# Kernel optimization log

Hardware: AMD Instinct MI355X
Metric: run time of the kernel (lower is better)

The kernel has to match this reference:

```python
import jax, jax.numpy as jnp
import numpy as np

B, L, D = 8, 1024, 1024
H = 16
HD = D // H  # 64
R = 8


def setup_inputs() -> dict:
    key = jax.random.key(0)
    ks = jax.random.split(key, 12)
    s = 1.0 / np.sqrt(D)
    return {
        "x": jax.random.normal(ks[0], (B, L, D), dtype=jnp.float32),
        "Wq": jax.random.normal(ks[1], (D, D), dtype=jnp.float32) * s,
        "bq": jnp.zeros((D,), dtype=jnp.float32),
        "Wk": jax.random.normal(ks[2], (D, D), dtype=jnp.float32) * s,
        "bk": jnp.zeros((D,), dtype=jnp.float32),
        "Wv": jax.random.normal(ks[3], (D, D), dtype=jnp.float32) * s,
        "bv": jnp.zeros((D,), dtype=jnp.float32),
        "Wo": jax.random.normal(ks[4], (D, D), dtype=jnp.float32) * s,
        "bo": jnp.zeros((D,), dtype=jnp.float32),
        "Wrel": jax.random.normal(ks[5], (H, R), dtype=jnp.float32) * (1.0 / np.sqrt(H)),
        "brel": jnp.zeros((R,), dtype=jnp.float32),
    }


def reference(x, Wq, bq, Wk, bk, Wv, bv, Wo, bo, Wrel, brel):
    # Standard MHA with need_weights=True: full [B,H,L,L] attention matrix.
    def heads(t):  # [B,L,D] -> [B,H,L,HD]
        return t.reshape(B, L, H, HD).transpose(0, 2, 1, 3)

    q = heads(x @ Wq + bq)
    k = heads(x @ Wk + bk)
    v = heads(x @ Wv + bv)

    scores = jnp.einsum('bhld,bhmd->bhlm', q, k) / jnp.sqrt(jnp.float32(HD))
    attn = jax.nn.softmax(scores, axis=-1)  # [B,H,L,L]

    ctx = jnp.einsum('bhlm,bhmd->bhld', attn, v)
    ctx = ctx.transpose(0, 2, 1, 3).reshape(B, L, D)
    output = ctx @ Wo + bo  # [B,L,D]

    # head_patterns: mean of attention weights over (L, L) -> [B, H]
    head_patterns = attn.mean(axis=(2, 3))
    relation_scores = head_patterns @ Wrel + brel  # [B,R]
    return output, relation_scores
```

## Files before the change

kernel.cpp:

```cpp
#include <hip/hip_runtime.h>
#include <math.h>

using f32x4  = __attribute__((ext_vector_type(4))) float;
using bf16x8 = __attribute__((ext_vector_type(8))) short;
using us8    = __attribute__((ext_vector_type(8))) unsigned short;
using us4    = __attribute__((ext_vector_type(4))) unsigned short;

static __device__ __forceinline__ unsigned short f32_bf16(float f) {
    unsigned int u = __float_as_uint(f);
    u += 0x7fffu + ((u >> 16) & 1u);
    return (unsigned short)(u >> 16);
}

static __device__ __forceinline__ float fast_exp2(float x) {
    return __builtin_amdgcn_exp2f(x);
}

static __device__ __forceinline__ unsigned int bf16pk(float lo, float hi) {
    unsigned int r;
    asm("v_cvt_pk_bf16_f32 %0, %1, %2" : "=v"(r) : "v"(lo), "v"(hi));
    return r;
}

#define GLOADLDS16(src, dst)                                                          \
    __builtin_amdgcn_global_load_lds(                                                 \
        (const __attribute__((address_space(1))) void*)(src),                         \
        (__attribute__((address_space(3))) void*)(dst), 16, 0, 0)

__global__ __launch_bounds__(256) void conv_x_kernel(const float* __restrict__ x,
                                                     unsigned short* __restrict__ xb) {
    const int i = blockIdx.x * 256 + threadIdx.x;
    const float4 v = ((const float4*)x)[i];
    us4 o;
    o.x = f32_bf16(v.x); o.y = f32_bf16(v.y); o.z = f32_bf16(v.z); o.w = f32_bf16(v.w);
    ((us4*)xb)[i] = o;
}

__global__ __launch_bounds__(256) void conv_wT_kernel(
    const float* __restrict__ Wq, const float* __restrict__ Wk,
    const float* __restrict__ Wv, const float* __restrict__ Wo,
    unsigned short* __restrict__ wqkvT, unsigned short* __restrict__ woT) {
    __shared__ float t[32][33];
    const int z = blockIdx.z;
    const float* W = (z == 0) ? Wq : (z == 1) ? Wk : (z == 2) ? Wv : Wo;
    unsigned short* dst = (z < 3) ? (wqkvT + (size_t)z * 1024 * 1024) : woT;
    const int bx = blockIdx.x * 32, by = blockIdx.y * 32;
    const int tx = threadIdx.x & 31, ty = threadIdx.x >> 5;
#pragma unroll
    for (int i = ty; i < 32; i += 8)
        t[i][tx] = W[(size_t)(by + i) * 1024 + bx + tx];
    __syncthreads();
#pragma unroll
    for (int i = ty; i < 32; i += 8)
        dst[(size_t)(bx + i) * 1024 + by + tx] = f32_bf16(t[tx][i]);
}

template<int MODE>
__global__ __launch_bounds__(256, 2) void gemm_bt_kernel(
    const unsigned short* __restrict__ A, const unsigned short* __restrict__ Bt,
    const float* __restrict__ bias_q, const float* __restrict__ bias_k,
    const float* __restrict__ bias_v,
    unsigned short* __restrict__ qkv, float* __restrict__ cout) {
    constexpr int K = 1024;
    __shared__ unsigned short As[256 * 64];
    __shared__ unsigned short Bs[128 * 64];
    const int tid = threadIdx.x;
    const int wid = tid >> 6, lane = tid & 63;
    const int bm = blockIdx.x * 256, bn = blockIdx.y * 128;
    const int wr = wid >> 1, wc = wid & 1;
    const int l15 = lane & 15, lg = lane >> 4;
    const int srow = lane >> 3;
    const int schunk = (lane & 7) ^ srow;

    f32x4 acc[8][4] = {};

    for (int kt = 0; kt < K / 64; ++kt) {
#pragma unroll
        for (int i = 0; i < 8; ++i) {
            const int li = wid * 8 + i;
            GLOADLDS16(A + (size_t)(bm + li * 8 + srow) * K + kt * 64 + schunk * 8,
                       &As[li * 512]);
        }
#pragma unroll
        for (int i = 0; i < 4; ++i) {
            const int li = wid * 4 + i;
            GLOADLDS16(Bt + (size_t)(bn + li * 8 + srow) * K + kt * 64 + schunk * 8,
                       &Bs[li * 512]);
        }
        __syncthreads();
#pragma unroll
        for (int ks = 0; ks < 2; ++ks) {
            bf16x8 bfr[4];
#pragma unroll
            for (int n = 0; n < 4; ++n) {
                const int row = wc * 64 + n * 16 + l15;
                const int c = (ks * 4 + lg) ^ (row & 7);
                bfr[n] = *(const bf16x8*)&Bs[row * 64 + c * 8];
            }
#pragma unroll
            for (int m = 0; m < 8; ++m) {
                const int row = wr * 128 + m * 16 + l15;
                const int c = (ks * 4 + lg) ^ (row & 7);
                const bf16x8 af = *(const bf16x8*)&As[row * 64 + c * 8];
#pragma unroll
                for (int n = 0; n < 4; ++n)
                    acc[m][n] = __builtin_amdgcn_mfma_f32_16x16x32_bf16(
                        bfr[n], af, acc[m][n], 0, 0, 0);
            }
        }
        __syncthreads();
    }
    if constexpr (MODE == 0) {
        const int which = bn >> 10;
        const int hnb = (bn & 1023) + wc * 64;
        const float* bias = (which == 0) ? bias_q : (which == 1) ? bias_k : bias_v;
        if (which == 2) {
#pragma unroll
            for (int m = 0; m < 8; ++m) {
                const int gm = bm + wr * 128 + m * 16 + l15;
                const int b_ = gm >> 10, li2 = gm & 1023;
#pragma unroll
                for (int n = 0; n < 4; ++n) {
                    const int hn0 = hnb + n * 16 + lg * 4;
                    const float4 bb = *(const float4*)&bias[hn0];
                    const float vv[4] = {acc[m][n][0] + bb.x, acc[m][n][1] + bb.y,
                                         acc[m][n][2] + bb.z, acc[m][n][3] + bb.w};
#pragma unroll
                    for (int r = 0; r < 4; ++r) {
                        const int hn = hn0 + r;
                        qkv[16777216 +
                            ((size_t)(b_ * 16 + (hn >> 6)) * 64 + (hn & 63)) * 1024 +
                            li2] = f32_bf16(vv[r]);
                    }
                }
            }
        } else {
            const float qs = (which == 0) ? 0.125f * 1.44269504088896f : 1.0f;
#pragma unroll
            for (int m = 0; m < 8; ++m) {
                const int gm = bm + wr * 128 + m * 16 + l15;
                const size_t rowbase =
                    (((size_t)which * 128 + (gm >> 10) * 16) * 1024 + (gm & 1023)) * 64;
#pragma unroll
                for (int n = 0; n < 4; ++n) {
                    const int hn0 = hnb + n * 16 + lg * 4;
                    const float4 bb = *(const float4*)&bias[hn0];
                    const unsigned int w01 = bf16pk((acc[m][n][0] + bb.x) * qs,
                                                    (acc[m][n][1] + bb.y) * qs);
                    const unsigned int w23 = bf16pk((acc[m][n][2] + bb.z) * qs,
                                                    (acc[m][n][3] + bb.w) * qs);
                    uint2 t2; t2.x = w01; t2.y = w23;
                    *(uint2*)&qkv[rowbase + (size_t)(hn0 >> 6) * 65536 + (hn0 & 63)] = t2;
                }
            }
        }
    } else {
#pragma unroll
        for (int m = 0; m < 8; ++m) {
            const int gm = bm + wr * 128 + m * 16 + l15;
#pragma unroll
            for (int n = 0; n < 4; ++n) {
                const int gn0 = bn + wc * 64 + n * 16 + lg * 4;
                const float4 bb = *(const float4*)&bias_q[gn0];
                float4 o;
                o.x = acc[m][n][0] + bb.x; o.y = acc[m][n][1] + bb.y;
                o.z = acc[m][n][2] + bb.z; o.w = acc[m][n][3] + bb.w;
                *(float4*)&cout[(size_t)gm * 1024 + gn0] = o;
            }
        }
    }
}

__global__ __launch_bounds__(512) void attn_kernel(
    const unsigned short* __restrict__ qkv, unsigned short* __restrict__ ctx) {
    __shared__ unsigned short Ks[2][4096];
    __shared__ unsigned short VTs[2][4096];
    __shared__ unsigned short Ps[8][1024];
    const int bh = blockIdx.x, qt = blockIdx.y;
    const int b = bh >> 4, h = bh & 15;
    const unsigned short* Qp  = qkv + (size_t)bh * 65536;
    const unsigned short* Kp  = qkv + 8388608  + (size_t)bh * 65536;
    const unsigned short* VTp = qkv + 16777216 + (size_t)bh * 65536;
    const int tid = threadIdx.x, wid = tid >> 6, lane = tid & 63;
    const int l15 = lane & 15, lg = lane >> 4;
    const int q0 = qt * 128 + wid * 16;
    const int srow = lane >> 3;
    const int schunk = (lane & 7) ^ srow;

    bf16x8 qf[2];
#pragma unroll
    for (int ks = 0; ks < 2; ++ks)
        qf[ks] = *(const bf16x8*)(Qp + (size_t)(q0 + l15) * 64 + ks * 32 + lg * 8);

    f32x4 oacc[4] = {};
    float lrow = 0.f;

    int koff[4][2], poff_r[2], poff_w[4];
#pragma unroll
    for (int nf = 0; nf < 4; ++nf)
#pragma unroll
        for (int ks = 0; ks < 2; ++ks) {
            const int row = nf * 16 + l15;
            koff[nf][ks] = row * 64 + (((ks * 4 + lg) ^ (row & 7)) * 8);
        }
#pragma unroll
    for (int ks = 0; ks < 2; ++ks)
        poff_r[ks] = l15 * 64 + (((ks * 4 + lg) ^ (l15 & 7)) * 8);
#pragma unroll
    for (int nf = 0; nf < 4; ++nf) {
        const int cchunk = nf * 2 + (lg >> 1);
        poff_w[nf] = l15 * 64 + ((cchunk ^ (l15 & 7)) * 8) + (lg & 1) * 4;
    }
    unsigned short* Pw = &Ps[wid][0];

#define ATTN_STAGE(KT, BB)                                                            \
    do {                                                                              \
        GLOADLDS16(Kp + (size_t)((KT) * 64 + wid * 8 + srow) * 64 + schunk * 8,       \
                   &Ks[BB][wid * 512]);                                               \
        GLOADLDS16(VTp + (size_t)(wid * 8 + srow) * 1024 + (KT) * 64 + schunk * 8,    \
                   &VTs[BB][wid * 512]);                                              \
    } while (0)

    ATTN_STAGE(0, 0);
    for (int kt = 0; kt < 16; ++kt) {
        const int cur = kt & 1;
        if (kt < 15) {
            ATTN_STAGE(kt + 1, cur ^ 1);
            asm volatile("s_waitcnt vmcnt(2)" ::: "memory");
        } else {
            asm volatile("s_waitcnt vmcnt(0)" ::: "memory");
        }
        __builtin_amdgcn_s_barrier();

        const unsigned short* Kb = &Ks[cur][0];
        const unsigned short* Vb = &VTs[cur][0];

        f32x4 sacc[4] = {};
        __builtin_amdgcn_s_setprio(1);
#pragma unroll
        for (int ks = 0; ks < 2; ++ks)
#pragma unroll
            for (int nf = 0; nf < 4; ++nf) {
                const bf16x8 kf = *(const bf16x8*)&Kb[koff[nf][ks]];
                sacc[nf] = __builtin_amdgcn_mfma_f32_16x16x32_bf16(
                    kf, qf[ks], sacc[nf], 0, 0, 0);
            }
        __builtin_amdgcn_s_setprio(0);

        float rsa = 0.f, rsb = 0.f;
#pragma unroll
        for (int nf = 0; nf < 4; ++nf) {
            const float p0 = fast_exp2(sacc[nf][0]);
            const float p1 = fast_exp2(sacc[nf][1]);
            const float p2 = fast_exp2(sacc[nf][2]);
            const float p3 = fast_exp2(sacc[nf][3]);
            rsa += p0 + p1; rsb += p2 + p3;
            uint2 t; t.x = bf16pk(p0, p1); t.y = bf16pk(p2, p3);
            *(uint2*)&Pw[poff_w[nf]] = t;
        }
        lrow += rsa + rsb;

        __builtin_amdgcn_s_setprio(1);
#pragma unroll
        for (int ks = 0; ks < 2; ++ks) {
            const bf16x8 pf = *(const bf16x8*)&Pw[poff_r[ks]];
#pragma unroll
            for (int nf = 0; nf < 4; ++nf) {
                const bf16x8 vf = *(const bf16x8*)&Vb[koff[nf][ks]];
                oacc[nf] = __builtin_amdgcn_mfma_f32_16x16x32_bf16(
                    vf, pf, oacc[nf], 0, 0, 0);
            }
        }
        __builtin_amdgcn_s_setprio(0);

        __builtin_amdgcn_s_barrier();
    }
#undef ATTN_STAGE

    lrow += __shfl_xor(lrow, 16);
    lrow += __shfl_xor(lrow, 32);
    const float rl = 1.0f / lrow;

#pragma unroll
    for (int nf = 0; nf < 4; ++nf) {
        uint2 t;
        t.x = bf16pk(oacc[nf][0] * rl, oacc[nf][1] * rl);
        t.y = bf16pk(oacc[nf][2] * rl, oacc[nf][3] * rl);
        *(uint2*)&ctx[((size_t)(b * 1024 + q0 + l15)) * 1024 + h * 64 + nf * 16 +
                      lg * 4] = t;
    }
}

__global__ __launch_bounds__(64) void relation_kernel(
    const float* __restrict__ Wrel, const float* __restrict__ brel,
    float* __restrict__ out) {
    const int t = threadIdx.x;
    const int r = t & 7;
    float s = 0.f;
#pragma unroll
    for (int hh = 0; hh < 16; ++hh) s += Wrel[hh * 8 + r];
    out[8 * 1024 * 1024 + t] = s * (1.0f / 1024.0f) + brel[r];
}

extern "C" void kernel_launch(void* const* d_in, const int* in_sizes, int n_in,
                              void* d_out, int out_size, void* d_ws, size_t ws_size,
                              hipStream_t stream) {
    (void)in_sizes; (void)n_in; (void)out_size; (void)ws_size;
    const float* x    = (const float*)d_in[0];
    const float* Wq   = (const float*)d_in[1];
    const float* bq   = (const float*)d_in[2];
    const float* Wk   = (const float*)d_in[3];
    const float* bk   = (const float*)d_in[4];
    const float* Wv   = (const float*)d_in[5];
    const float* bv   = (const float*)d_in[6];
    const float* Wo   = (const float*)d_in[7];
    const float* bo   = (const float*)d_in[8];
    const float* Wrel = (const float*)d_in[9];
    const float* brel = (const float*)d_in[10];
    float* out = (float*)d_out;

    char* ws = (char*)d_ws;
    unsigned short* xb    = (unsigned short*)ws;
    unsigned short* wqkvT = (unsigned short*)(ws + 16777216);
    unsigned short* woT   = (unsigned short*)(ws + 16777216 + 6291456);
    unsigned short* qkv   = (unsigned short*)(ws + 16777216 + 6291456 + 2097152);
    unsigned short* ctx   = xb;

    conv_x_kernel<<<8192, 256, 0, stream>>>(x, xb);
    conv_wT_kernel<<<dim3(32, 32, 4), 256, 0, stream>>>(Wq, Wk, Wv, Wo, wqkvT, woT);
    gemm_bt_kernel<0><<<dim3(32, 24), 256, 0, stream>>>(
        xb, wqkvT, bq, bk, bv, qkv, nullptr);
    attn_kernel<<<dim3(128, 8), 512, 0, stream>>>(qkv, ctx);
    gemm_bt_kernel<1><<<dim3(32, 8), 256, 0, stream>>>(
        ctx, woT, bo, nullptr, nullptr, nullptr, out);
    relation_kernel<<<1, 64, 0, stream>>>(Wrel, brel, out);
}
```

Measured before the change: 162.8 us.

## Process two query sub-tiles per wave in attention to reuse K/V fragments

The attention kernel now runs 4 waves per block instead of 8, and each wave handles 32 query rows as two 16-row sub-tiles. Each K and V^T fragment read from LDS feeds two MFMAs, which halves LDS fragment traffic per unit of compute. Each wave now issues two global-to-LDS loads per stage, so the wait count is raised to match. The cost is more accumulator registers per wave and fewer waves per block, which launch_bounds(256,2) tries to offset by allowing two blocks per CU.

```diff
diff --git a/kernel.cpp b/kernel.cpp
--- a/kernel.cpp
+++ b/kernel.cpp
@@ -171,11 +171,11 @@
     }
 }
 
-__global__ __launch_bounds__(512) void attn_kernel(
+__global__ __launch_bounds__(256, 2) void attn_kernel(
     const unsigned short* __restrict__ qkv, unsigned short* __restrict__ ctx) {
     __shared__ unsigned short Ks[2][4096];
     __shared__ unsigned short VTs[2][4096];
-    __shared__ unsigned short Ps[8][1024];
+    __shared__ unsigned short Ps[4][2][1024];
     const int bh = blockIdx.x, qt = blockIdx.y;
     const int b = bh >> 4, h = bh & 15;
     const unsigned short* Qp  = qkv + (size_t)bh * 65536;
@@ -183,17 +183,20 @@
     const unsigned short* VTp = qkv + 16777216 + (size_t)bh * 65536;
     const int tid = threadIdx.x, wid = tid >> 6, lane = tid & 63;
     const int l15 = lane & 15, lg = lane >> 4;
-    const int q0 = qt * 128 + wid * 16;
+    const int q0 = qt * 128 + wid * 32;
     const int srow = lane >> 3;
     const int schunk = (lane & 7) ^ srow;
 
-    bf16x8 qf[2];
-#pragma unroll
-    for (int ks = 0; ks < 2; ++ks)
-        qf[ks] = *(const bf16x8*)(Qp + (size_t)(q0 + l15) * 64 + ks * 32 + lg * 8);
-
-    f32x4 oacc[4] = {};
-    float lrow = 0.f;
+    bf16x8 qf[2][2];
+#pragma unroll
+    for (int s = 0; s < 2; ++s)
+#pragma unroll
+        for (int ks = 0; ks < 2; ++ks)
+            qf[s][ks] = *(const bf16x8*)(Qp + (size_t)(q0 + s * 16 + l15) * 64 +
+                                         ks * 32 + lg * 8);
+
+    f32x4 oacc[2][4] = {};
+    float lrow[2] = {0.f, 0.f};
 
     int koff[4][2], poff_r[2], poff_w[4];
 #pragma unroll
@@ -211,14 +214,17 @@
         const int cchunk = nf * 2 + (lg >> 1);
         poff_w[nf] = l15 * 64 + ((cchunk ^ (l15 & 7)) * 8) + (lg & 1) * 4;
     }
-    unsigned short* Pw = &Ps[wid][0];
 
 #define ATTN_STAGE(KT, BB)                                                            \
     do {                                                                              \
-        GLOADLDS16(Kp + (size_t)((KT) * 64 + wid * 8 + srow) * 64 + schunk * 8,       \
-                   &Ks[BB][wid * 512]);                                               \
-        GLOADLDS16(VTp + (size_t)(wid * 8 + srow) * 1024 + (KT) * 64 + schunk * 8,    \
-                   &VTs[BB][wid * 512]);                                              \
+        _Pragma("unroll")                                                             \
+        for (int i = 0; i < 2; ++i) {                                                 \
+            const int li = wid * 2 + i;                                               \
+            GLOADLDS16(Kp + (size_t)((KT) * 64 + li * 8 + srow) * 64 + schunk * 8,    \
+                       &Ks[BB][li * 512]);                                            \
+            GLOADLDS16(VTp + (size_t)(li * 8 + srow) * 1024 + (KT) * 64 + schunk * 8, \
+                       &VTs[BB][li * 512]);                                           \
+        }                                                                             \
     } while (0)
 
     ATTN_STAGE(0, 0);
@@ -226,7 +232,7 @@
         const int cur = kt & 1;
         if (kt < 15) {
             ATTN_STAGE(kt + 1, cur ^ 1);
-            asm volatile("s_waitcnt vmcnt(2)" ::: "memory");
+            asm volatile("s_waitcnt vmcnt(4)" ::: "memory");
         } else {
             asm volatile("s_waitcnt vmcnt(0)" ::: "memory");
         }
@@ -235,40 +241,49 @@
         const unsigned short* Kb = &Ks[cur][0];
         const unsigned short* Vb = &VTs[cur][0];
 
-        f32x4 sacc[4] = {};
+        f32x4 sacc[2][4] = {};
         __builtin_amdgcn_s_setprio(1);
 #pragma unroll
         for (int ks = 0; ks < 2; ++ks)
 #pragma unroll
             for (int nf = 0; nf < 4; ++nf) {
                 const bf16x8 kf = *(const bf16x8*)&Kb[koff[nf][ks]];
-                sacc[nf] = __builtin_amdgcn_mfma_f32_16x16x32_bf16(
-                    kf, qf[ks], sacc[nf], 0, 0, 0);
+                sacc[0][nf] = __builtin_amdgcn_mfma_f32_16x16x32_bf16(
+                    kf, qf[0][ks], sacc[0][nf], 0, 0, 0);
+                sacc[1][nf] = __builtin_amdgcn_mfma_f32_16x16x32_bf16(
+                    kf, qf[1][ks], sacc[1][nf], 0, 0, 0);
             }
         __builtin_amdgcn_s_setprio(0);
 
-        float rsa = 0.f, rsb = 0.f;
-#pragma unroll
-        for (int nf = 0; nf < 4; ++nf) {
-            const float p0 = fast_exp2(sacc[nf][0]);
-            const float p1 = fast_exp2(sacc[nf][1]);
-            const float p2 = fast_exp2(sacc[nf][2]);
-            const float p3 = fast_exp2(sacc[nf][3]);
-            rsa += p0 + p1; rsb += p2 + p3;
-            uint2 t; t.x = bf16pk(p0, p1); t.y = bf16pk(p2, p3);
-            *(uint2*)&Pw[poff_w[nf]] = t;
-        }
-        lrow += rsa + rsb;
+#pragma unroll
+        for (int s = 0; s < 2; ++s) {
+            unsigned short* Pw = &Ps[wid][s][0];
+            float rsa = 0.f, rsb = 0.f;
+#pragma unroll
+            for (int nf = 0; nf < 4; ++nf) {
+                const float p0 = fast_exp2(sacc[s][nf][0]);
+                const float p1 = fast_exp2(sacc[s][nf][1]);
+                const float p2 = fast_exp2(sacc[s][nf][2]);
+                const float p3 = fast_exp2(sacc[s][nf][3]);
+                rsa += p0 + p1; rsb += p2 + p3;
+                uint2 t; t.x = bf16pk(p0, p1); t.y = bf16pk(p2, p3);
+                *(uint2*)&Pw[poff_w[nf]] = t;
+            }
+            lrow[s] += rsa + rsb;
+        }
 
         __builtin_amdgcn_s_setprio(1);
 #pragma unroll
         for (int ks = 0; ks < 2; ++ks) {
-            const bf16x8 pf = *(const bf16x8*)&Pw[poff_r[ks]];
+            const bf16x8 pf0 = *(const bf16x8*)&Ps[wid][0][poff_r[ks]];
+            const bf16x8 pf1 = *(const bf16x8*)&Ps[wid][1][poff_r[ks]];
 #pragma unroll
             for (int nf = 0; nf < 4; ++nf) {
                 const bf16x8 vf = *(const bf16x8*)&Vb[koff[nf][ks]];
-                oacc[nf] = __builtin_amdgcn_mfma_f32_16x16x32_bf16(
-                    vf, pf, oacc[nf], 0, 0, 0);
+                oacc[0][nf] = __builtin_amdgcn_mfma_f32_16x16x32_bf16(
+                    vf, pf0, oacc[0][nf], 0, 0, 0);
+                oacc[1][nf] = __builtin_amdgcn_mfma_f32_16x16x32_bf16(
+                    vf, pf1, oacc[1][nf], 0, 0, 0);
             }
         }
         __builtin_amdgcn_s_setprio(0);
@@ -277,17 +292,20 @@
     }
 #undef ATTN_STAGE
 
-    lrow += __shfl_xor(lrow, 16);
-    lrow += __shfl_xor(lrow, 32);
-    const float rl = 1.0f / lrow;
-
-#pragma unroll
-    for (int nf = 0; nf < 4; ++nf) {
-        uint2 t;
-        t.x = bf16pk(oacc[nf][0] * rl, oacc[nf][1] * rl);
-        t.y = bf16pk(oacc[nf][2] * rl, oacc[nf][3] * rl);
-        *(uint2*)&ctx[((size_t)(b * 1024 + q0 + l15)) * 1024 + h * 64 + nf * 16 +
-                      lg * 4] = t;
+#pragma unroll
+    for (int s = 0; s < 2; ++s) {
+        float l = lrow[s];
+        l += __shfl_xor(l, 16);
+        l += __shfl_xor(l, 32);
+        const float rl = 1.0f / l;
+#pragma unroll
+        for (int nf = 0; nf < 4; ++nf) {
+            uint2 t;
+            t.x = bf16pk(oacc[s][nf][0] * rl, oacc[s][nf][1] * rl);
+            t.y = bf16pk(oacc[s][nf][2] * rl, oacc[s][nf][3] * rl);
+            *(uint2*)&ctx[((size_t)(b * 1024 + q0 + s * 16 + l15)) * 1024 + h * 64 +
+                          nf * 16 + lg * 4] = t;
+        }
     }
 }
 
@@ -330,7 +348,7 @@
     conv_wT_kernel<<<dim3(32, 32, 4), 256, 0, stream>>>(Wq, Wk, Wv, Wo, wqkvT, woT);
     gemm_bt_kernel<0><<<dim3(32, 24), 256, 0, stream>>>(
         xb, wqkvT, bq, bk, bv, qkv, nullptr);
-    attn_kernel<<<dim3(128, 8), 512, 0, stream>>>(qkv, ctx);
+    attn_kernel<<<dim3(128, 8), 256, 0, stream>>>(qkv, ctx);
     gemm_bt_kernel<1><<<dim3(32, 8), 256, 0, stream>>>(
         ctx, woT, bo, nullptr, nullptr, nullptr, out);
     relation_kernel<<<1, 64, 0, stream>>>(Wrel, brel, out);
```

New measurement: 161.6 us. Within noise of the previous version (-0.7%).
